# Kernel tuning notes

Hardware: AMD Instinct MI355X
Metric: run time of the kernel (lower is better)

The kernel has to match this reference:

```python
import jax, jax.numpy as jnp
import numpy as np

ANGLE = 0.5  # angular margin from init_kwargs


def setup_inputs() -> dict:
    key = jax.random.key(0)
    k1, k2, k3 = jax.random.split(key, 3)
    B, F, C = 512, 128, 100000
    # scale by 0.1 so exp(features @ w) and exp(modulus * cos) stay finite in fp32
    features = jax.random.normal(k1, (B, F), dtype=jnp.float32) * 0.1
    w = jax.random.normal(k2, (F, C), dtype=jnp.float32) * 0.1
    target = jax.random.randint(k3, (B,), 0, C, dtype=jnp.int64)
    return {"features": features, "w": w, "target": target}


def reference(features, w, target):
    B = features.shape[0]
    rows = jnp.arange(B)
    # norms: [B,1] and [1,C]
    features_modulus = jnp.sqrt(jnp.sum(features ** 2, axis=1, keepdims=True))
    w_modulus = jnp.sqrt(jnp.sum(w ** 2, axis=0, keepdims=True))
    modulus = features_modulus * w_modulus  # [B, C]
    logits = jnp.matmul(features, w)  # [B, C] (computed once; torch computes it twice)
    cos_theta = logits / modulus / 1.01
    theta = jnp.arccos(cos_theta) + ANGLE
    cos_theta_plus = jnp.cos(theta)
    margin_logits = modulus * cos_theta_plus  # [B, C]
    top = jnp.exp(margin_logits[rows, target])  # [B]
    down_ = jnp.exp(logits)  # [B, C]
    down = jnp.sum(down_, axis=1) - down_[rows, target] + top  # [B]
    return -jnp.sum(jnp.log(top / down)) / B
```

## Files before the change

### kernel.cpp

```cpp
#include <hip/hip_runtime.h>

#define F_DIM 128
#define C_DIM 100000
#define B_ROWS 512
#define ANGLE 0.5f
#define NXB 196
#define COLS_PER_BLK 512

typedef __attribute__((ext_vector_type(4))) float  f32x4;
typedef __attribute__((ext_vector_type(8))) short  bf16x8;
typedef __attribute__((ext_vector_type(4))) short  bf16x4;

static __device__ __forceinline__ unsigned short f2bf(float x) {
    unsigned int u = __float_as_uint(x);
    u += 0x7FFFu + ((u >> 16) & 1u);
    return (unsigned short)(u >> 16);
}

__global__ __launch_bounds__(256, 2)
void arc_main(const float* __restrict__ feat,
              const float* __restrict__ w,
              float* __restrict__ pp)
{
    __shared__ unsigned short lA[128 * 128];
    __shared__ unsigned short lB[128 * 128];
    __shared__ float lRow[128];

    const int tid    = threadIdx.x;
    const int r0     = blockIdx.x * 128;
    const int cblk   = blockIdx.y;
    const int cbase0 = cblk * COLS_PER_BLK;

    if (tid < 128) lRow[tid] = 0.f;

    #pragma unroll
    for (int it = 0; it < 16; ++it) {
        const int idx4 = it * 256 + tid;
        const int row  = idx4 >> 5;
        const int c4   = idx4 & 31;
        const f32x4 v  = *(const f32x4*)(feat + (size_t)(r0 + row) * F_DIM + c4 * 4);
        bf16x4 h;
        h[0] = (short)f2bf(v[0]); h[1] = (short)f2bf(v[1]);
        h[2] = (short)f2bf(v[2]); h[3] = (short)f2bf(v[3]);
        const int pc   = (c4 >> 1) ^ (row & 15);
        const int half = c4 & 1;
        *(bf16x4*)&lA[row * 128 + pc * 8 + half * 4] = h;
    }

    const int lane = tid & 63;
    const int wv   = tid >> 6;
    const int quad = lane >> 4;
    const int l15  = lane & 15;
    const int nb   = wv * 32;

    float esum[8][4];
    #pragma unroll
    for (int m = 0; m < 8; ++m)
        #pragma unroll
        for (int r = 0; r < 4; ++r) esum[m][r] = 0.f;

    for (int t = 0; t < 4; ++t) {
        const int cbase = cbase0 + t * 128;

        #pragma unroll
        for (int it = 0; it < 16; ++it) {
            const int idx4 = it * 256 + tid;
            const int k    = idx4 >> 5;
            const int c4   = idx4 & 31;
            const int c    = cbase + c4 * 4;
            f32x4 v = {0.f, 0.f, 0.f, 0.f};
            if (c < C_DIM)
                v = *(const f32x4*)(w + (size_t)k * C_DIM + c);
            bf16x4 h;
            h[0] = (short)f2bf(v[0]); h[1] = (short)f2bf(v[1]);
            h[2] = (short)f2bf(v[2]); h[3] = (short)f2bf(v[3]);
            *(bf16x4*)&lB[k * 128 + c4 * 4] = h;
        }
        __syncthreads();

        f32x4 acc[8][2];
        #pragma unroll
        for (int m = 0; m < 8; ++m) {
            acc[m][0] = (f32x4){0.f, 0.f, 0.f, 0.f};
            acc[m][1] = (f32x4){0.f, 0.f, 0.f, 0.f};
        }

        #pragma unroll
        for (int ks = 0; ks < 4; ++ks) {
            bf16x8 bfr[2];
            #pragma unroll
            for (int s = 0; s < 2; ++s) {
                #pragma unroll
                for (int j = 0; j < 8; ++j)
                    bfr[s][j] = (short)lB[(ks * 32 + quad * 8 + j) * 128 + nb + s * 16 + l15];
            }
            #pragma unroll
            for (int m = 0; m < 8; ++m) {
                const int row = m * 16 + l15;
                const int pc  = (ks * 4 + quad) ^ (row & 15);
                const bf16x8 af = *(const bf16x8*)&lA[row * 128 + pc * 8];
                acc[m][0] = __builtin_amdgcn_mfma_f32_16x16x32_bf16(af, bfr[0], acc[m][0], 0, 0, 0);
                acc[m][1] = __builtin_amdgcn_mfma_f32_16x16x32_bf16(af, bfr[1], acc[m][1], 0, 0, 0);
            }
        }

        const int  col0 = cbase + nb + l15;
        const int  col1 = col0 + 16;
        const bool v0   = col0 < C_DIM;
        const bool v1   = col1 < C_DIM;
        #pragma unroll
        for (int m = 0; m < 8; ++m) {
            #pragma unroll
            for (int r = 0; r < 4; ++r) {
                if (v0) esum[m][r] += __expf(acc[m][0][r]);
                if (v1) esum[m][r] += __expf(acc[m][1][r]);
            }
        }
        __syncthreads();
    }

    #pragma unroll
    for (int m = 0; m < 8; ++m) {
        #pragma unroll
        for (int r = 0; r < 4; ++r) {
            float s = esum[m][r];
            #pragma unroll
            for (int off = 1; off < 16; off <<= 1)
                s += __shfl_xor(s, off);
            if (l15 == 0)
                atomicAdd(&lRow[m * 16 + quad * 4 + r], s);
        }
    }
    __syncthreads();
    if (tid < 128)
        pp[(size_t)(r0 + tid) * NXB + cblk] = lRow[tid];
}

__global__ void arc_row(const float* __restrict__ feat,
                        const float* __restrict__ w,
                        const int*   __restrict__ target,
                        const float* __restrict__ pp,
                        float* __restrict__ term)
{
    const int b    = blockIdx.x;
    const int lane = threadIdx.x;
    const int t    = target[b];

    float dot = 0.f, wsq = 0.f, fsq = 0.f, rs = 0.f;
    #pragma unroll
    for (int h = 0; h < 2; ++h) {
        const int f  = lane + h * 64;
        const float fv = feat[b * F_DIM + f];
        const float wv = w[(size_t)f * C_DIM + t];
        dot += fv * wv;
        wsq += wv * wv;
        fsq += fv * fv;
    }
    for (int j = lane; j < NXB; j += 64)
        rs += pp[(size_t)b * NXB + j];

    #pragma unroll
    for (int off = 32; off > 0; off >>= 1) {
        dot += __shfl_xor(dot, off);
        wsq += __shfl_xor(wsq, off);
        fsq += __shfl_xor(fsq, off);
        rs  += __shfl_xor(rs,  off);
    }
    if (lane == 0) {
        const float mod = sqrtf(fsq) * sqrtf(wsq);
        float ct = dot / (mod * 1.01f);
        ct = fminf(1.f, fmaxf(-1.f, ct));
        const float th   = acosf(ct) + ANGLE;
        const float marg = mod * cosf(th);
        const float down = rs - expf(dot) + expf(marg);
        term[b] = marg - logf(down);
    }
}

__global__ void arc_loss(const float* __restrict__ term,
                         float* __restrict__ out)
{
    __shared__ float red[B_ROWS];
    const int b = threadIdx.x;
    red[b] = term[b];
    __syncthreads();
    #pragma unroll
    for (int st = 256; st > 0; st >>= 1) {
        if (b < st) red[b] += red[b + st];
        __syncthreads();
    }
    if (b == 0) out[0] = -red[0] / (float)B_ROWS;
}

extern "C" void kernel_launch(void* const* d_in, const int* in_sizes, int n_in,
                              void* d_out, int out_size, void* d_ws, size_t ws_size,
                              hipStream_t stream)
{
    const float* feat   = (const float*)d_in[0];
    const float* w      = (const float*)d_in[1];
    const int*   target = (const int*)d_in[2];

    float* pp   = (float*)d_ws;
    float* term = pp + (size_t)B_ROWS * NXB;

    arc_main<<<dim3(4, NXB), 256, 0, stream>>>(feat, w, pp);
    arc_row<<<B_ROWS, 64, 0, stream>>>(feat, w, target, pp, term);
    arc_loss<<<1, B_ROWS, 0, stream>>>(term, (float*)d_out);
}
```

Before: 144.0 us.

## Fuse row and loss kernels into main via last-block reduction, prefetch W tiles

Merges the per-row margin kernel and the final loss reduction into the main GEMM kernel. An atomic counter picks the last block to finish, and that block computes all 512 row terms and the mean. W tiles are prefetched into registers one step ahead of the LDS store, and the LDS row stride for B is padded to 130 to reduce bank conflicts. This removes two kernel launches and overlaps the global loads with MFMA work. In exchange it adds a memset launch, raises register pressure from the 16-vector prefetch buffer, and makes the tail serial: a single block does all 512 rows, each thread with 128 strided W loads and 196 partial-sum loads.

```diff
diff --git a/kernel.cpp b/kernel.cpp
--- a/kernel.cpp
+++ b/kernel.cpp
@@ -5,7 +5,8 @@
 #define B_ROWS 512
 #define ANGLE 0.5f
 #define NXB 196
-#define COLS_PER_BLK 512
+#define NBLK (4 * NXB)
+#define LBS 130
 
 typedef __attribute__((ext_vector_type(4))) float  f32x4;
 typedef __attribute__((ext_vector_type(8))) short  bf16x8;
@@ -18,18 +19,22 @@
 }
 
 __global__ __launch_bounds__(256, 2)
-void arc_main(const float* __restrict__ feat,
-              const float* __restrict__ w,
-              float* __restrict__ pp)
+void arc_fused(const float* __restrict__ feat,
+               const float* __restrict__ w,
+               const int*   __restrict__ target,
+               float* __restrict__ pp,
+               unsigned* counter,
+               float* __restrict__ out)
 {
     __shared__ unsigned short lA[128 * 128];
-    __shared__ unsigned short lB[128 * 128];
+    __shared__ unsigned short lB[128 * LBS];
     __shared__ float lRow[128];
+    __shared__ unsigned lastFlag;
 
     const int tid    = threadIdx.x;
     const int r0     = blockIdx.x * 128;
     const int cblk   = blockIdx.y;
-    const int cbase0 = cblk * COLS_PER_BLK;
+    const int cbase0 = cblk * 512;
 
     if (tid < 128) lRow[tid] = 0.f;
 
@@ -42,9 +47,8 @@
         bf16x4 h;
         h[0] = (short)f2bf(v[0]); h[1] = (short)f2bf(v[1]);
         h[2] = (short)f2bf(v[2]); h[3] = (short)f2bf(v[3]);
-        const int pc   = (c4 >> 1) ^ (row & 15);
-        const int half = c4 & 1;
-        *(bf16x4*)&lA[row * 128 + pc * 8 + half * 4] = h;
+        const int pc = (c4 >> 1) ^ (row & 15);
+        *(bf16x4*)&lA[row * 128 + pc * 8 + (c4 & 1) * 4] = h;
     }
 
     const int lane = tid & 63;
@@ -52,6 +56,8 @@
     const int quad = lane >> 4;
     const int l15  = lane & 15;
     const int nb   = wv * 32;
+    const int sc4  = tid & 31;
+    const int sk0  = tid >> 5;
 
     float esum[8][4];
     #pragma unroll
@@ -59,24 +65,37 @@
         #pragma unroll
         for (int r = 0; r < 4; ++r) esum[m][r] = 0.f;
 
+    f32x4 pre[16];
+    {
+        const int c = cbase0 + sc4 * 4;
+        #pragma unroll
+        for (int it = 0; it < 16; ++it) {
+            pre[it] = (f32x4){0.f, 0.f, 0.f, 0.f};
+            if (c < C_DIM)
+                pre[it] = *(const f32x4*)(w + (size_t)(it * 8 + sk0) * C_DIM + c);
+        }
+    }
+
+    #pragma unroll
     for (int t = 0; t < 4; ++t) {
-        const int cbase = cbase0 + t * 128;
-
         #pragma unroll
         for (int it = 0; it < 16; ++it) {
-            const int idx4 = it * 256 + tid;
-            const int k    = idx4 >> 5;
-            const int c4   = idx4 & 31;
-            const int c    = cbase + c4 * 4;
-            f32x4 v = {0.f, 0.f, 0.f, 0.f};
-            if (c < C_DIM)
-                v = *(const f32x4*)(w + (size_t)k * C_DIM + c);
             bf16x4 h;
-            h[0] = (short)f2bf(v[0]); h[1] = (short)f2bf(v[1]);
-            h[2] = (short)f2bf(v[2]); h[3] = (short)f2bf(v[3]);
-            *(bf16x4*)&lB[k * 128 + c4 * 4] = h;
+            h[0] = (short)f2bf(pre[it][0]); h[1] = (short)f2bf(pre[it][1]);
+            h[2] = (short)f2bf(pre[it][2]); h[3] = (short)f2bf(pre[it][3]);
+            *(bf16x4*)&lB[(it * 8 + sk0) * LBS + sc4 * 4] = h;
         }
         __syncthreads();
+
+        if (t < 3) {
+            const int c = cbase0 + (t + 1) * 128 + sc4 * 4;
+            #pragma unroll
+            for (int it = 0; it < 16; ++it) {
+                pre[it] = (f32x4){0.f, 0.f, 0.f, 0.f};
+                if (c < C_DIM)
+                    pre[it] = *(const f32x4*)(w + (size_t)(it * 8 + sk0) * C_DIM + c);
+            }
+        }
 
         f32x4 acc[8][2];
         #pragma unroll
@@ -84,7 +103,6 @@
             acc[m][0] = (f32x4){0.f, 0.f, 0.f, 0.f};
             acc[m][1] = (f32x4){0.f, 0.f, 0.f, 0.f};
         }
-
         #pragma unroll
         for (int ks = 0; ks < 4; ++ks) {
             bf16x8 bfr[2];
@@ -92,7 +110,7 @@
             for (int s = 0; s < 2; ++s) {
                 #pragma unroll
                 for (int j = 0; j < 8; ++j)
-                    bfr[s][j] = (short)lB[(ks * 32 + quad * 8 + j) * 128 + nb + s * 16 + l15];
+                    bfr[s][j] = (short)lB[(ks * 32 + quad * 8 + j) * LBS + nb + s * 16 + l15];
             }
             #pragma unroll
             for (int m = 0; m < 8; ++m) {
@@ -104,7 +122,7 @@
             }
         }
 
-        const int  col0 = cbase + nb + l15;
+        const int  col0 = cbase0 + t * 128 + nb + l15;
         const int  col1 = col0 + 16;
         const bool v0   = col0 < C_DIM;
         const bool v1   = col1 < C_DIM;
@@ -132,64 +150,54 @@
         }
     }
     __syncthreads();
+
     if (tid < 128)
-        pp[(size_t)(r0 + tid) * NXB + cblk] = lRow[tid];
-}
-
-__global__ void arc_row(const float* __restrict__ feat,
-                        const float* __restrict__ w,
-                        const int*   __restrict__ target,
-                        const float* __restrict__ pp,
-                        float* __restrict__ term)
-{
-    const int b    = blockIdx.x;
-    const int lane = threadIdx.x;
-    const int t    = target[b];
-
-    float dot = 0.f, wsq = 0.f, fsq = 0.f, rs = 0.f;
-    #pragma unroll
-    for (int h = 0; h < 2; ++h) {
-        const int f  = lane + h * 64;
-        const float fv = feat[b * F_DIM + f];
-        const float wv = w[(size_t)f * C_DIM + t];
-        dot += fv * wv;
-        wsq += wv * wv;
-        fsq += fv * fv;
-    }
-    for (int j = lane; j < NXB; j += 64)
-        rs += pp[(size_t)b * NXB + j];
-
-    #pragma unroll
-    for (int off = 32; off > 0; off >>= 1) {
-        dot += __shfl_xor(dot, off);
-        wsq += __shfl_xor(wsq, off);
-        fsq += __shfl_xor(fsq, off);
-        rs  += __shfl_xor(rs,  off);
-    }
-    if (lane == 0) {
+        __hip_atomic_store(pp + (size_t)cblk * 512 + r0 + tid, lRow[tid],
+                           __ATOMIC_RELAXED, __HIP_MEMORY_SCOPE_AGENT);
+    __threadfence();
+    __syncthreads();
+    if (tid == 0) {
+        unsigned prev = __hip_atomic_fetch_add(counter, 1u,
+                            __ATOMIC_ACQ_REL, __HIP_MEMORY_SCOPE_AGENT);
+        lastFlag = (prev == NBLK - 1) ? 1u : 0u;
+    }
+    __syncthreads();
+    if (lastFlag == 0u) return;
+    __threadfence();
+
+    float* lT = (float*)lA;
+    #pragma unroll
+    for (int rr = 0; rr < 2; ++rr) {
+        const int b = tid + rr * 256;
+        const int tg = target[b];
+        float dot = 0.f, fsq = 0.f, wsq = 0.f;
+        #pragma unroll 8
+        for (int f = 0; f < F_DIM; ++f) {
+            const float fv = feat[b * F_DIM + f];
+            const float wvv = w[(size_t)f * C_DIM + tg];
+            dot += fv * wvv; fsq += fv * fv; wsq += wvv * wvv;
+        }
+        float rs = 0.f;
+        for (int j = 0; j < NXB; ++j)
+            rs += __hip_atomic_load(pp + (size_t)j * 512 + b,
+                                    __ATOMIC_RELAXED, __HIP_MEMORY_SCOPE_AGENT);
         const float mod = sqrtf(fsq) * sqrtf(wsq);
         float ct = dot / (mod * 1.01f);
         ct = fminf(1.f, fmaxf(-1.f, ct));
         const float th   = acosf(ct) + ANGLE;
         const float marg = mod * cosf(th);
         const float down = rs - expf(dot) + expf(marg);
-        term[b] = marg - logf(down);
-    }
-}
-
-__global__ void arc_loss(const float* __restrict__ term,
-                         float* __restrict__ out)
-{
-    __shared__ float red[B_ROWS];
-    const int b = threadIdx.x;
-    red[b] = term[b];
-    __syncthreads();
-    #pragma unroll
-    for (int st = 256; st > 0; st >>= 1) {
-        if (b < st) red[b] += red[b + st];
+        lT[b] = marg - logf(down);
+    }
+    __syncthreads();
+    lT[tid] += lT[tid + 256];
+    __syncthreads();
+    #pragma unroll
+    for (int st = 128; st > 0; st >>= 1) {
+        if (tid < st) lT[tid] += lT[tid + st];
         __syncthreads();
     }
-    if (b == 0) out[0] = -red[0] / (float)B_ROWS;
+    if (tid == 0) out[0] = -lT[0] / (float)B_ROWS;
 }
 
 extern "C" void kernel_launch(void* const* d_in, const int* in_sizes, int n_in,
@@ -200,10 +208,10 @@
     const float* w      = (const float*)d_in[1];
     const int*   target = (const int*)d_in[2];
 
-    float* pp   = (float*)d_ws;
-    float* term = pp + (size_t)B_ROWS * NXB;
-
-    arc_main<<<dim3(4, NXB), 256, 0, stream>>>(feat, w, pp);
-    arc_row<<<B_ROWS, 64, 0, stream>>>(feat, w, target, pp, term);
-    arc_loss<<<1, B_ROWS, 0, stream>>>(term, (float*)d_out);
+    float*    pp      = (float*)d_ws;
+    unsigned* counter = (unsigned*)(pp + (size_t)NXB * 512);
+
+    hipMemsetAsync(counter, 0, sizeof(unsigned), stream);
+    arc_fused<<<dim3(4, NXB), 256, 0, stream>>>(feat, w, target, pp, counter,
+                                                (float*)d_out);
 }
```

Result: slower. 337.4 us (+134.3%).
